# Optimization experiments

Measured on AMD Instinct MI355X. Metric: run time of the kernel, lower is better.

The kernel has to match this reference:

```python
import jax, jax.numpy as jnp
import numpy as np

D = 512
O = 64

def setup_inputs() -> dict:
    key = jax.random.key(0)
    k1, k2, k3, k4 = jax.random.split(key, 4)
    B, N, F, V = 4, 1024, 16, 64
    x = jax.random.normal(k1, (B, N, D), dtype=jnp.float32)
    idx = jax.random.randint(k2, (B, F), 0, V)
    feature_bias_table = jax.random.normal(k3, (V, D), dtype=jnp.float32)
    out_projection_table = jax.random.normal(k4, (V, D * O), dtype=jnp.float32) * (1.0 / np.sqrt(D))
    return {"x": x, "idx": idx, "feature_bias_table": feature_bias_table,
            "out_projection_table": out_projection_table}

def reference(x, idx, feature_bias_table, out_projection_table):
    # x: [B,N,D], idx: [B,F]
    w = out_projection_table[idx].reshape(*idx.shape, D, O)   # [B,F,D,O]
    b = feature_bias_table[idx]                               # [B,F,D]
    xb = x[:, :, None, :] + b[:, None, :, :]                  # [B,N,F,D]
    out = jnp.einsum('bnfd,bfdo->bnfo', xb, w)                # [B,N,F,O]
    return out
```

## Files before the change

### kernel.cpp

```cpp
#include <hip/hip_runtime.h>
#include <hip/hip_bf16.h>
#include <stdint.h>


typedef __bf16 bf16_t;
typedef __bf16 bf16x8 __attribute__((ext_vector_type(8)));
typedef float floatx4 __attribute__((ext_vector_type(4)));

__device__ __forceinline__ void async_ld16(const bf16_t* g, bf16_t* l) {
    __builtin_amdgcn_global_load_lds(
        (const __attribute__((address_space(1))) void*)g,
        (__attribute__((address_space(3))) void*)l,
        16, 0, 0);
}

__global__ __launch_bounds__(256) void prep_kernel(
    const float* __restrict__ w,
    const float* __restrict__ bias,
    const float* __restrict__ x,
    bf16_t* __restrict__ wt,
    float* __restrict__ cv,
    bf16_t* __restrict__ xb)
{
    const int t = threadIdx.x;
    if (blockIdx.x >= 64) {
        const int base = (blockIdx.x - 64) * 2048 + t * 8;
        const float4 f0 = *(const float4*)(x + base);
        const float4 f1 = *(const float4*)(x + base + 4);
        bf16x8 o;
        o[0] = (bf16_t)f0.x; o[1] = (bf16_t)f0.y;
        o[2] = (bf16_t)f0.z; o[3] = (bf16_t)f0.w;
        o[4] = (bf16_t)f1.x; o[5] = (bf16_t)f1.y;
        o[6] = (bf16_t)f1.z; o[7] = (bf16_t)f1.w;
        *(bf16x8*)(xb + base) = o;
        return;
    }

    const int v = blockIdx.x;
    __shared__ float tile[64][68];
    __shared__ float bch[64];
    __shared__ float red[4][64];

    const int r  = t >> 2, cs = (t & 3) * 16;
    const int o  = t >> 2, ds = (t & 3) * 16;
    const int dq = t >> 6, oc = t & 63;
    float csum = 0.f;

    for (int c = 0; c < 8; ++c) {
        __syncthreads();
        const float* src = w + (size_t)v * 32768 + (size_t)(c * 64 + r) * 64 + cs;
        *(float4*)&tile[r][cs]      = *(const float4*)(src);
        *(float4*)&tile[r][cs + 4]  = *(const float4*)(src + 4);
        *(float4*)&tile[r][cs + 8]  = *(const float4*)(src + 8);
        *(float4*)&tile[r][cs + 12] = *(const float4*)(src + 12);
        if (t < 64) bch[t] = bias[v * 512 + c * 64 + t];
        __syncthreads();

        bf16x8 t0, t1;
#pragma unroll
        for (int j = 0; j < 8; ++j) t0[j] = (bf16_t)tile[ds + j][o];
#pragma unroll
        for (int j = 0; j < 8; ++j) t1[j] = (bf16_t)tile[ds + 8 + j][o];
        bf16_t* dst = wt + ((size_t)v * 64 + o) * 512 + c * 64 + ds;
        *(bf16x8*)&dst[0] = t0;
        *(bf16x8*)&dst[8] = t1;

#pragma unroll
        for (int j = 0; j < 16; ++j) {
            const int dl = dq * 16 + j;
            csum += bch[dl] * tile[dl][oc];
        }
    }
    red[dq][oc] = csum;
    __syncthreads();
    if (t < 64) cv[v * 64 + t] = red[0][t] + red[1][t] + red[2][t] + red[3][t];
}

__global__ __launch_bounds__(256, 2) void gemm_kernel(
    const bf16_t* __restrict__ xb,
    const bf16_t* __restrict__ wt,
    const float*  __restrict__ cv,
    const int*    __restrict__ idx,
    float* __restrict__ out)
{
    const int bid = blockIdx.x;
    const int f  = bid & 15;
    const int mt = (bid >> 4) & 7;
    const int b  = bid >> 7;
    const int v  = idx[b * 16 + f];

    const int tid  = threadIdx.x;
    const int lane = tid & 63;
    const int wave = tid >> 6;
    const int wm = wave >> 1;
    const int wn = wave & 1;
    const int l15 = lane & 15;
    const int l4  = lane >> 4;

    const bf16_t* Ag = xb + (size_t)(b * 1024 + mt * 128) * 512;
    const bf16_t* Bg = wt + (size_t)v * 64 * 512;

    __shared__ __align__(16) bf16_t As[2][128 * 32];
    __shared__ __align__(16) bf16_t Bs[2][64 * 32];

    floatx4 acc[4][2] = {};

    const int ar0 = tid >> 2;
    const int ar1 = (tid + 256) >> 2;
    const int aq  = (tid & 3) * 8;
    const int br  = tid >> 2;
    const int bq  = (tid & 3) * 8;

    async_ld16(Ag + ar0 * 512 + aq, &As[0][tid * 8]);
    async_ld16(Ag + ar1 * 512 + aq, &As[0][(tid + 256) * 8]);
    async_ld16(Bg + br * 512 + bq, &Bs[0][tid * 8]);

    for (int kk = 0; kk < 16; ++kk) {
        const int buf = kk & 1;
        __syncthreads();
        if (kk < 15) {
            const int k0 = (kk + 1) * 32;
            async_ld16(Ag + ar0 * 512 + k0 + aq, &As[buf ^ 1][tid * 8]);
            async_ld16(Ag + ar1 * 512 + k0 + aq, &As[buf ^ 1][(tid + 256) * 8]);
            async_ld16(Bg + br * 512 + k0 + bq, &Bs[buf ^ 1][tid * 8]);
        }
        bf16x8 a[4], bb[2];
#pragma unroll
        for (int mi = 0; mi < 4; ++mi)
            a[mi] = *(const bf16x8*)&As[buf][(wm * 64 + mi * 16 + l15) * 32 + l4 * 8];
#pragma unroll
        for (int ni = 0; ni < 2; ++ni)
            bb[ni] = *(const bf16x8*)&Bs[buf][(wn * 32 + ni * 16 + l15) * 32 + l4 * 8];
#pragma unroll
        for (int mi = 0; mi < 4; ++mi)
#pragma unroll
            for (int ni = 0; ni < 2; ++ni)
                acc[mi][ni] = __builtin_amdgcn_mfma_f32_16x16x32_bf16(
                    a[mi], bb[ni], acc[mi][ni], 0, 0, 0);
    }

    const int colbase = wn * 32 + l15;
    const float c0 = cv[v * 64 + colbase];
    const float c1 = cv[v * 64 + colbase + 16];
    float* outp = out + (size_t)(b * 1024 + mt * 128 + wm * 64 + l4 * 4) * 1024
                      + f * 64;
#pragma unroll
    for (int mi = 0; mi < 4; ++mi) {
#pragma unroll
        for (int r = 0; r < 4; ++r) {
            float* row = outp + (size_t)(mi * 16 + r) * 1024;
            row[colbase]      = acc[mi][0][r] + c0;
            row[colbase + 16] = acc[mi][1][r] + c1;
        }
    }
}

__global__ __launch_bounds__(256) void naive_kernel(
    const float* __restrict__ x, const float* __restrict__ w,
    const float* __restrict__ bias, const int* __restrict__ idx,
    float* __restrict__ out)
{
    const int b = blockIdx.x >> 10;
    const int n = blockIdx.x & 1023;
    __shared__ float xr[512];
    for (int d = threadIdx.x; d < 512; d += 256)
        xr[d] = x[(size_t)(b * 1024 + n) * 512 + d];
    __syncthreads();
    for (int p = threadIdx.x; p < 1024; p += 256) {
        const int f = p >> 6, o = p & 63;
        const int v = idx[b * 16 + f];
        const float* wp = w + (size_t)v * 32768 + o;
        const float* bp = bias + v * 512;
        float s = 0.f;
        for (int d = 0; d < 512; ++d)
            s += (xr[d] + bp[d]) * wp[(size_t)d * 64];
        out[(size_t)(b * 1024 + n) * 1024 + p] = s;
    }
}

extern "C" void kernel_launch(void* const* d_in, const int* in_sizes, int n_in,
                              void* d_out, int out_size, void* d_ws, size_t ws_size,
                              hipStream_t stream) {
    const float* x    = (const float*)d_in[0];
    const int*   idx  = (const int*)d_in[1];
    const float* bias = (const float*)d_in[2];
    const float* w    = (const float*)d_in[3];
    float* out = (float*)d_out;

    const size_t cv_bytes = 64 * 64 * sizeof(float);
    const size_t wt_bytes = (size_t)64 * 64 * 512 * 2;
    const size_t xb_bytes = (size_t)4096 * 512 * 2;
    if (ws_size >= cv_bytes + wt_bytes + xb_bytes) {
        float*  cv = (float*)d_ws;
        bf16_t* wt = (bf16_t*)((char*)d_ws + cv_bytes);
        bf16_t* xb = (bf16_t*)((char*)d_ws + cv_bytes + wt_bytes);
        prep_kernel<<<1088, 256, 0, stream>>>(w, bias, x, wt, cv, xb);
        gemm_kernel<<<512, 256, 0, stream>>>(xb, wt, cv, idx, out);
    } else {
        naive_kernel<<<4096, 256, 0, stream>>>(x, w, bias, idx, out);
    }
}
```

Baseline: 95.95 us.

## Double K-tile to 64 with XOR-swizzled LDS, remap blocks, prefetch prep tiles

The GEMM kernel now stages 64-wide K tiles instead of 32, halving the number of barrier-separated iterations. It XOR-swizzles the LDS layout to avoid bank conflicts on fragment reads. It reorders the block-to-(f,b,mt) mapping so consecutive blocks share the same weight slice, and raises the launch-bounds occupancy hint to 3. The prep kernel register-prefetches the next weight tile during the transpose, overlapping global loads with LDS work. The cost is larger LDS use per block, which may conflict with the higher occupancy target.

```diff
diff --git a/kernel.cpp b/kernel.cpp
--- a/kernel.cpp
+++ b/kernel.cpp
@@ -45,17 +45,31 @@
     const int o  = t >> 2, ds = (t & 3) * 16;
     const int dq = t >> 6, oc = t & 63;
     float csum = 0.f;
-
+    const float* wv = w + (size_t)v * 32768;
+
+    float4 rg0, rg1, rg2, rg3;
+    {
+        const float* src = wv + (size_t)r * 64 + cs;
+        rg0 = *(const float4*)(src);
+        rg1 = *(const float4*)(src + 4);
+        rg2 = *(const float4*)(src + 8);
+        rg3 = *(const float4*)(src + 12);
+    }
     for (int c = 0; c < 8; ++c) {
         __syncthreads();
-        const float* src = w + (size_t)v * 32768 + (size_t)(c * 64 + r) * 64 + cs;
-        *(float4*)&tile[r][cs]      = *(const float4*)(src);
-        *(float4*)&tile[r][cs + 4]  = *(const float4*)(src + 4);
-        *(float4*)&tile[r][cs + 8]  = *(const float4*)(src + 8);
-        *(float4*)&tile[r][cs + 12] = *(const float4*)(src + 12);
+        *(float4*)&tile[r][cs]      = rg0;
+        *(float4*)&tile[r][cs + 4]  = rg1;
+        *(float4*)&tile[r][cs + 8]  = rg2;
+        *(float4*)&tile[r][cs + 12] = rg3;
         if (t < 64) bch[t] = bias[v * 512 + c * 64 + t];
         __syncthreads();
-
+        if (c < 7) {
+            const float* src = wv + (size_t)((c + 1) * 64 + r) * 64 + cs;
+            rg0 = *(const float4*)(src);
+            rg1 = *(const float4*)(src + 4);
+            rg2 = *(const float4*)(src + 8);
+            rg3 = *(const float4*)(src + 12);
+        }
         bf16x8 t0, t1;
 #pragma unroll
         for (int j = 0; j < 8; ++j) t0[j] = (bf16_t)tile[ds + j][o];
@@ -64,7 +78,6 @@
         bf16_t* dst = wt + ((size_t)v * 64 + o) * 512 + c * 64 + ds;
         *(bf16x8*)&dst[0] = t0;
         *(bf16x8*)&dst[8] = t1;
-
 #pragma unroll
         for (int j = 0; j < 16; ++j) {
             const int dl = dq * 16 + j;
@@ -76,7 +89,7 @@
     if (t < 64) cv[v * 64 + t] = red[0][t] + red[1][t] + red[2][t] + red[3][t];
 }
 
-__global__ __launch_bounds__(256, 2) void gemm_kernel(
+__global__ __launch_bounds__(256, 3) void gemm_kernel(
     const bf16_t* __restrict__ xb,
     const bf16_t* __restrict__ wt,
     const float*  __restrict__ cv,
@@ -84,9 +97,9 @@
     float* __restrict__ out)
 {
     const int bid = blockIdx.x;
-    const int f  = bid & 15;
-    const int mt = (bid >> 4) & 7;
-    const int b  = bid >> 7;
+    const int f  = bid >> 5;
+    const int b  = (bid >> 3) & 3;
+    const int mt = bid & 7;
     const int v  = idx[b * 16 + f];
 
     const int tid  = threadIdx.x;
@@ -100,43 +113,73 @@
     const bf16_t* Ag = xb + (size_t)(b * 1024 + mt * 128) * 512;
     const bf16_t* Bg = wt + (size_t)v * 64 * 512;
 
-    __shared__ __align__(16) bf16_t As[2][128 * 32];
-    __shared__ __align__(16) bf16_t Bs[2][64 * 32];
+    __shared__ __align__(16) bf16_t As[2][128 * 64];
+    __shared__ __align__(16) bf16_t Bs[2][64 * 64];
 
     floatx4 acc[4][2] = {};
 
-    const int ar0 = tid >> 2;
-    const int ar1 = (tid + 256) >> 2;
-    const int aq  = (tid & 3) * 8;
-    const int br  = tid >> 2;
-    const int bq  = (tid & 3) * 8;
-
-    async_ld16(Ag + ar0 * 512 + aq, &As[0][tid * 8]);
-    async_ld16(Ag + ar1 * 512 + aq, &As[0][(tid + 256) * 8]);
-    async_ld16(Bg + br * 512 + bq, &Bs[0][tid * 8]);
-
-    for (int kk = 0; kk < 16; ++kk) {
+    int a_row[4], a_col[4];
+#pragma unroll
+    for (int j = 0; j < 4; ++j) {
+        const int s = tid + 256 * j;
+        a_row[j] = s >> 3;
+        a_col[j] = ((s & 7) ^ (a_row[j] & 7)) * 8;
+    }
+    int b_row[2], b_col[2];
+#pragma unroll
+    for (int j = 0; j < 2; ++j) {
+        const int s = tid + 256 * j;
+        b_row[j] = s >> 3;
+        b_col[j] = ((s & 7) ^ (b_row[j] & 7)) * 8;
+    }
+
+#pragma unroll
+    for (int j = 0; j < 4; ++j)
+        async_ld16(Ag + a_row[j] * 512 + a_col[j], &As[0][(tid + 256 * j) * 8]);
+#pragma unroll
+    for (int j = 0; j < 2; ++j)
+        async_ld16(Bg + b_row[j] * 512 + b_col[j], &Bs[0][(tid + 256 * j) * 8]);
+
+    for (int kk = 0; kk < 8; ++kk) {
         const int buf = kk & 1;
         __syncthreads();
-        if (kk < 15) {
-            const int k0 = (kk + 1) * 32;
-            async_ld16(Ag + ar0 * 512 + k0 + aq, &As[buf ^ 1][tid * 8]);
-            async_ld16(Ag + ar1 * 512 + k0 + aq, &As[buf ^ 1][(tid + 256) * 8]);
-            async_ld16(Bg + br * 512 + k0 + bq, &Bs[buf ^ 1][tid * 8]);
-        }
-        bf16x8 a[4], bb[2];
+        if (kk < 7) {
+            const int k0 = (kk + 1) * 64;
+#pragma unroll
+            for (int j = 0; j < 4; ++j)
+                async_ld16(Ag + a_row[j] * 512 + k0 + a_col[j],
+                           &As[buf ^ 1][(tid + 256 * j) * 8]);
+#pragma unroll
+            for (int j = 0; j < 2; ++j)
+                async_ld16(Bg + b_row[j] * 512 + k0 + b_col[j],
+                           &Bs[buf ^ 1][(tid + 256 * j) * 8]);
+        }
+        bf16x8 a[4][2], bb[2][2];
+#pragma unroll
+        for (int mi = 0; mi < 4; ++mi) {
+            const int row = wm * 64 + mi * 16 + l15;
+#pragma unroll
+            for (int ks = 0; ks < 2; ++ks)
+                a[mi][ks] = *(const bf16x8*)
+                    &As[buf][row * 64 + (((ks * 4 + l4) ^ (row & 7)) * 8)];
+        }
+#pragma unroll
+        for (int ni = 0; ni < 2; ++ni) {
+            const int row = wn * 32 + ni * 16 + l15;
+#pragma unroll
+            for (int ks = 0; ks < 2; ++ks)
+                bb[ni][ks] = *(const bf16x8*)
+                    &Bs[buf][row * 64 + (((ks * 4 + l4) ^ (row & 7)) * 8)];
+        }
 #pragma unroll
         for (int mi = 0; mi < 4; ++mi)
-            a[mi] = *(const bf16x8*)&As[buf][(wm * 64 + mi * 16 + l15) * 32 + l4 * 8];
-#pragma unroll
-        for (int ni = 0; ni < 2; ++ni)
-            bb[ni] = *(const bf16x8*)&Bs[buf][(wn * 32 + ni * 16 + l15) * 32 + l4 * 8];
-#pragma unroll
-        for (int mi = 0; mi < 4; ++mi)
-#pragma unroll
-            for (int ni = 0; ni < 2; ++ni)
+#pragma unroll
+            for (int ni = 0; ni < 2; ++ni) {
                 acc[mi][ni] = __builtin_amdgcn_mfma_f32_16x16x32_bf16(
-                    a[mi], bb[ni], acc[mi][ni], 0, 0, 0);
+                    a[mi][0], bb[ni][0], acc[mi][ni], 0, 0, 0);
+                acc[mi][ni] = __builtin_amdgcn_mfma_f32_16x16x32_bf16(
+                    a[mi][1], bb[ni][1], acc[mi][ni], 0, 0, 0);
+            }
     }
 
     const int colbase = wn * 32 + l15;
```

After: 89.96 us. 6.2% less time.
